# Performance work log

Measured on AMD Instinct MI355X. Metric: run time of the kernel, lower is better.

Reference implementation:

```python
import jax, jax.numpy as jnp
import numpy as np

D_MODEL = 768
NHEAD = 12
D_K = D_MODEL // NHEAD
D_FF = 3072
EPS = 1e-6


def layer_norm(x, a, b):
    # torch LayerNorm here: mean/std over last dim, std is UNBIASED (n-1), eps added to std
    n = x.shape[-1]
    m = jnp.mean(x, axis=-1, keepdims=True)
    var = jnp.sum((x - m) ** 2, axis=-1, keepdims=True) / (n - 1)
    return a * (x - m) / (jnp.sqrt(var) + EPS) + b


def setup_inputs() -> dict:
    key = jax.random.key(0)
    ks = jax.random.split(key, 12)
    B, S = 2, 2048
    s = 1.0 / np.sqrt(D_MODEL)
    inp = {
        'x': jax.random.normal(ks[0], (B, S, D_MODEL), jnp.float32),
        'mask': jnp.ones((B, 1, S), jnp.int32),
        'Wq': jax.random.normal(ks[1], (D_MODEL, D_MODEL), jnp.float32) * s,
        'bq': jnp.zeros((D_MODEL,), jnp.float32),
        'Wk': jax.random.normal(ks[2], (D_MODEL, D_MODEL), jnp.float32) * s,
        'bk': jnp.zeros((D_MODEL,), jnp.float32),
        'Wv': jax.random.normal(ks[3], (D_MODEL, D_MODEL), jnp.float32) * s,
        'bv': jnp.zeros((D_MODEL,), jnp.float32),
        'Wo': jax.random.normal(ks[4], (D_MODEL, D_MODEL), jnp.float32) * s,
        'bo': jnp.zeros((D_MODEL,), jnp.float32),
        'ln1_a': jnp.ones((D_MODEL,), jnp.float32),
        'ln1_b': jnp.zeros((D_MODEL,), jnp.float32),
        'W1': jax.random.normal(ks[5], (D_MODEL, D_FF), jnp.float32) * s,
        'b1': jnp.zeros((D_FF,), jnp.float32),
        'W2': jax.random.normal(ks[6], (D_FF, D_MODEL), jnp.float32) * (1.0 / np.sqrt(D_FF)),
        'b2': jnp.zeros((D_MODEL,), jnp.float32),
        'ln2_a': jnp.ones((D_MODEL,), jnp.float32),
        'ln2_b': jnp.zeros((D_MODEL,), jnp.float32),
    }
    return inp


def reference(x, mask, Wq, bq, Wk, bk, Wv, bv, Wo, bo, ln1_a, ln1_b, W1, b1, W2, b2, ln2_a, ln2_b):
    B, S, _ = x.shape
    # --- sublayer 1: pre-norm self-attention + residual (dropout = eval/no-op) ---
    h = layer_norm(x, ln1_a, ln1_b)
    q = (h @ Wq + bq).reshape(B, S, NHEAD, D_K).transpose(0, 2, 1, 3)  # [B,H,S,Dk]
    k = (h @ Wk + bk).reshape(B, S, NHEAD, D_K).transpose(0, 2, 1, 3)
    v = (h @ Wv + bv).reshape(B, S, NHEAD, D_K).transpose(0, 2, 1, 3)
    scores = jnp.einsum('bhqd,bhkd->bhqk', q, k) / np.sqrt(D_K)  # [B,H,S,S]
    scores = jnp.where(mask[:, None] == 0, jnp.float32(-1e9), scores)
    attn = jax.nn.softmax(scores, axis=-1)
    ctx = jnp.einsum('bhqk,bhkd->bhqd', attn, v)  # [B,H,S,Dk]
    ctx = ctx.transpose(0, 2, 1, 3).reshape(B, S, D_MODEL)
    x = x + (ctx @ Wo + bo)
    # --- sublayer 2: pre-norm FFN + residual ---
    h2 = layer_norm(x, ln2_a, ln2_b)
    ff = jax.nn.relu(h2 @ W1 + b1) @ W2 + b2
    return x + ff
```

## Files before the change

### kernel.cpp

```cpp
#include <hip/hip_runtime.h>
#include <hip/hip_bf16.h>
#include <stdint.h>

#define DM 768
#define DFF 3072
#define NH 12
#define DK 64
#define SS 2048
#define NTOK 4096
#define KCH 2

typedef __hip_bfloat16 bf16;
typedef short bf16x8 __attribute__((ext_vector_type(8)));
typedef float f32x4 __attribute__((ext_vector_type(4)));

#define MFMA16(a, b, c) __builtin_amdgcn_mfma_f32_16x16x32_bf16((a), (b), (c), 0, 0, 0)

#define QSCALE 0.18033688011112042f

#if __has_builtin(__builtin_amdgcn_exp2f)
#define EXP2F(x) __builtin_amdgcn_exp2f(x)
#else
#define EXP2F(x) exp2f(x)
#endif

static __device__ __forceinline__ bf16 f2b(float f) { return __float2bfloat16(f); }
static __device__ __forceinline__ unsigned short f2b_bits(float f) {
    bf16 h = __float2bfloat16(f);
    return *reinterpret_cast<unsigned short*>(&h);
}
static __device__ __forceinline__ float b2f(bf16 h) { return __bfloat162float(h); }

static __device__ __forceinline__ void g2l16(const void* g, void* l) {
    __builtin_amdgcn_global_load_lds(
        (const __attribute__((address_space(1))) unsigned int*)g,
        (__attribute__((address_space(3))) unsigned int*)(uintptr_t)l,
        16, 0, 0);
}

__global__ __launch_bounds__(256) void transpose_all(const float* Wq, const float* Wk,
                                                     const float* Wv, const float* Wo,
                                                     const float* W1, const float* W2,
                                                     bf16* WqT, bf16* WkT, bf16* WvT,
                                                     bf16* WoT, bf16* W1T, bf16* W2T) {
    __shared__ float tile[32][33];
    int id = blockIdx.x;
    const float* W; bf16* WT; int K, N, n0, k0;
    if (id < 2304) {
        int z = id / 576, r = id % 576;
        W  = (z == 0) ? Wq : (z == 1) ? Wk : (z == 2) ? Wv : Wo;
        WT = (z == 0) ? WqT : (z == 1) ? WkT : (z == 2) ? WvT : WoT;
        K = 768; N = 768; n0 = (r % 24) * 32; k0 = (r / 24) * 32;
    } else if (id < 4608) {
        int r = id - 2304; W = W1; WT = W1T;
        K = 768; N = 3072; n0 = (r % 96) * 32; k0 = (r / 96) * 32;
    } else {
        int r = id - 4608; W = W2; WT = W2T;
        K = 3072; N = 768; n0 = (r % 24) * 32; k0 = (r / 24) * 32;
    }
    int tx = threadIdx.x & 31, ty = threadIdx.x >> 5;
#pragma unroll
    for (int r = ty; r < 32; r += 8)
        tile[r][tx] = W[(size_t)(k0 + r) * N + n0 + tx];
    __syncthreads();
#pragma unroll
    for (int r = ty; r < 32; r += 8)
        WT[(size_t)(n0 + r) * K + k0 + tx] = f2b(tile[tx][r]);
}

__global__ __launch_bounds__(256) void ln_fwd(const float* __restrict__ x,
                                              const float* __restrict__ g,
                                              const float* __restrict__ be,
                                              bf16* __restrict__ out) {
    int wid = threadIdx.x >> 6, lane = threadIdx.x & 63;
    int row = blockIdx.x * 4 + wid;
    const float* xr = x + (size_t)row * DM;
    float v[12];
    float s = 0.f;
#pragma unroll
    for (int i = 0; i < 12; ++i) { v[i] = xr[lane + i * 64]; s += v[i]; }
#pragma unroll
    for (int off = 32; off >= 1; off >>= 1) s += __shfl_xor(s, off);
    float mean = s * (1.f / 768.f);
    float s2 = 0.f;
#pragma unroll
    for (int i = 0; i < 12; ++i) { float d = v[i] - mean; s2 += d * d; }
#pragma unroll
    for (int off = 32; off >= 1; off >>= 1) s2 += __shfl_xor(s2, off);
    float rstd = 1.f / (sqrtf(s2 * (1.f / 767.f)) + 1e-6f);
    bf16* orow = out + (size_t)row * DM;
#pragma unroll
    for (int i = 0; i < 12; ++i) {
        int c = lane + i * 64;
        orow[c] = f2b(g[c] * (v[i] - mean) * rstd + be[c]);
    }
}

__device__ __forceinline__ void gemm_core(const bf16* __restrict__ A,
                                          const bf16* __restrict__ BT,
                                          int K, int bm, int bn,
                                          bf16* As, bf16* Bs,
                                          f32x4 acc[4][4]) {
    int tid = threadIdx.x;
    int lane = tid & 63, quad = lane >> 4, lid = lane & 15;
    int wid = tid >> 6;
    int wm = (wid >> 1) * 64, wn = (wid & 1) * 64;
    int s0 = tid, s1 = tid + 256;
    int r0 = s0 >> 2, c0 = (s0 & 3) ^ ((r0 >> 1) & 3);
    int r1 = s1 >> 2, c1 = (s1 & 3) ^ ((r1 >> 1) & 3);
    const bf16* A0 = A + (size_t)(bm + r0) * K + c0 * 8;
    const bf16* A1 = A + (size_t)(bm + r1) * K + c1 * 8;
    const bf16* B0 = BT + (size_t)(bn + r0) * K + c0 * 8;
    const bf16* B1 = BT + (size_t)(bn + r1) * K + c1 * 8;
    int rdc = quad ^ ((lid >> 1) & 3);
    g2l16(A0, As + s0 * 8);
    g2l16(B0, Bs + s0 * 8);
    g2l16(A1, As + s1 * 8);
    g2l16(B1, Bs + s1 * 8);
    for (int k0 = 0; k0 < K; k0 += 32) {
        __syncthreads();
        int cur = (k0 >> 5) & 1;
        if (k0 + 32 < K) {
            int nb = (cur ^ 1) * 4096;
            g2l16(A0 + k0 + 32, As + nb + s0 * 8);
            g2l16(B0 + k0 + 32, Bs + nb + s0 * 8);
            g2l16(A1 + k0 + 32, As + nb + s1 * 8);
            g2l16(B1 + k0 + 32, Bs + nb + s1 * 8);
        }
        const bf16* Ac = As + cur * 4096;
        const bf16* Bc = Bs + cur * 4096;
        bf16x8 af[4], bfr[4];
#pragma unroll
        for (int i = 0; i < 4; ++i) af[i]  = *(const bf16x8*)&Ac[(wm + i * 16 + lid) * 32 + rdc * 8];
#pragma unroll
        for (int j = 0; j < 4; ++j) bfr[j] = *(const bf16x8*)&Bc[(wn + j * 16 + lid) * 32 + rdc * 8];
#pragma unroll
        for (int i = 0; i < 4; ++i)
#pragma unroll
            for (int j = 0; j < 4; ++j)
                acc[i][j] = MFMA16(af[i], bfr[j], acc[i][j]);
    }
}

__global__ __launch_bounds__(256) void gemm_qkv(const bf16* __restrict__ A,
                                                const bf16* __restrict__ WqT,
                                                const bf16* __restrict__ WkT,
                                                const bf16* __restrict__ WvT,
                                                const float* __restrict__ bq,
                                                const float* __restrict__ bk,
                                                const float* __restrict__ bv,
                                                bf16* __restrict__ qb,
                                                bf16* __restrict__ kb,
                                                bf16* __restrict__ vtb) {
    __shared__ bf16 As[2 * 128 * 32];
    __shared__ bf16 Bs[2 * 128 * 32];
    int which = blockIdx.x / 6;
    int bn = (blockIdx.x % 6) * 128;
    int bm = blockIdx.y * 128;
    const bf16* BT = (which == 0) ? WqT : (which == 1) ? WkT : WvT;
    const float* bias = (which == 0) ? bq : (which == 1) ? bk : bv;
    f32x4 acc[4][4] = {};
    gemm_core(A, BT, DM, bm, bn, As, Bs, acc);

    int tid = threadIdx.x, wid = tid >> 6, lane = tid & 63, quad = lane >> 4, lid = lane & 15;
    int wm = (wid >> 1) * 64, wn = (wid & 1) * 64;
    float sc = (which == 0) ? QSCALE : 1.f;
#pragma unroll
    for (int j = 0; j < 4; ++j) {
        int col = bn + wn + j * 16 + lid;
        float bb = bias[col];
        int hh = col >> 6, d = col & 63;
#pragma unroll
        for (int i = 0; i < 4; ++i) {
            int rowbase = bm + wm + i * 16 + quad * 4;
            int b = rowbase >> 11;
            int s0 = rowbase & 2047;
            if (which == 2) {
                ushort4 pk;
                pk.x = f2b_bits(acc[i][j][0] + bb);
                pk.y = f2b_bits(acc[i][j][1] + bb);
                pk.z = f2b_bits(acc[i][j][2] + bb);
                pk.w = f2b_bits(acc[i][j][3] + bb);
                *(ushort4*)&vtb[(((size_t)b * NH + hh) * DK + d) * SS + s0] = pk;
            } else {
                bf16* dst = which ? kb : qb;
#pragma unroll
                for (int r = 0; r < 4; ++r)
                    dst[(((size_t)b * NH + hh) * SS + (s0 + r)) * DK + d] = f2b((acc[i][j][r] + bb) * sc);
            }
        }
    }
}

template <int EPI>
__global__ __launch_bounds__(256) void gemm_ep(const bf16* __restrict__ A,
                                               const bf16* __restrict__ BT,
                                               const float* __restrict__ bias,
                                               const float* __restrict__ res,
                                               void* __restrict__ outp,
                                               int N, int K) {
    __shared__ bf16 As[2 * 128 * 32];
    __shared__ bf16 Bs[2 * 128 * 32];
    int bm = blockIdx.y * 128, bn = blockIdx.x * 128;
    f32x4 acc[4][4] = {};
    gemm_core(A, BT, K, bm, bn, As, Bs, acc);

    int tid = threadIdx.x, wid = tid >> 6, lane = tid & 63, quad = lane >> 4, lid = lane & 15;
    int wm = (wid >> 1) * 64, wn = (wid & 1) * 64;
#pragma unroll
    for (int j = 0; j < 4; ++j) {
        int col = bn + wn + j * 16 + lid;
        float bb = bias[col];
#pragma unroll
        for (int i = 0; i < 4; ++i) {
#pragma unroll
            for (int r = 0; r < 4; ++r) {
                int row = bm + wm + i * 16 + quad * 4 + r;
                float v = acc[i][j][r] + bb;
                if (EPI == 2) {
                    ((float*)outp)[(size_t)row * N + col] = res[(size_t)row * N + col] + v;
                } else {
                    ((bf16*)outp)[(size_t)row * N + col] = f2b(fmaxf(v, 0.f));
                }
            }
        }
    }
}

template <int EPI>
__global__ __launch_bounds__(256) void gemm_ep64(const bf16* __restrict__ A,
                                                 const bf16* __restrict__ BT,
                                                 const float* __restrict__ bias,
                                                 const float* __restrict__ res,
                                                 void* __restrict__ outp,
                                                 int N, int K) {
    __shared__ bf16 As[2 * 64 * 32];
    __shared__ bf16 Bs[2 * 128 * 32];
    int bm = blockIdx.y * 64, bn = blockIdx.x * 128;
    int tid = threadIdx.x, wid = tid >> 6, lane = tid & 63, quad = lane >> 4, lid = lane & 15;
    int wm = (wid >> 1) * 32, wn = (wid & 1) * 64;
    f32x4 acc[2][4] = {};
    int ra = tid >> 2, ca = (tid & 3) ^ ((ra >> 1) & 3);
    int s0 = tid, s1 = tid + 256;
    int rb0 = s0 >> 2, cb0 = (s0 & 3) ^ ((rb0 >> 1) & 3);
    int rb1 = s1 >> 2, cb1 = (s1 & 3) ^ ((rb1 >> 1) & 3);
    const bf16* Ap = A + (size_t)(bm + ra) * K + ca * 8;
    const bf16* B0 = BT + (size_t)(bn + rb0) * K + cb0 * 8;
    const bf16* B1 = BT + (size_t)(bn + rb1) * K + cb1 * 8;
    int rdc = quad ^ ((lid >> 1) & 3);
    g2l16(Ap, As + tid * 8);
    g2l16(B0, Bs + s0 * 8);
    g2l16(B1, Bs + s1 * 8);
    for (int k0 = 0; k0 < K; k0 += 32) {
        __syncthreads();
        int cur = (k0 >> 5) & 1;
        if (k0 + 32 < K) {
            g2l16(Ap + k0 + 32, As + (cur ^ 1) * 2048 + tid * 8);
            g2l16(B0 + k0 + 32, Bs + (cur ^ 1) * 4096 + s0 * 8);
            g2l16(B1 + k0 + 32, Bs + (cur ^ 1) * 4096 + s1 * 8);
        }
        const bf16* Ac = As + cur * 2048;
        const bf16* Bc = Bs + cur * 4096;
        bf16x8 af[2], bfr[4];
#pragma unroll
        for (int i = 0; i < 2; ++i) af[i]  = *(const bf16x8*)&Ac[(wm + i * 16 + lid) * 32 + rdc * 8];
#pragma unroll
        for (int j = 0; j < 4; ++j) bfr[j] = *(const bf16x8*)&Bc[(wn + j * 16 + lid) * 32 + rdc * 8];
#pragma unroll
        for (int i = 0; i < 2; ++i)
#pragma unroll
            for (int j = 0; j < 4; ++j)
                acc[i][j] = MFMA16(af[i], bfr[j], acc[i][j]);
    }
#pragma unroll
    for (int j = 0; j < 4; ++j) {
        int col = bn + wn + j * 16 + lid;
        float bb = bias[col];
#pragma unroll
        for (int i = 0; i < 2; ++i) {
#pragma unroll
            for (int r = 0; r < 4; ++r) {
                int row = bm + wm + i * 16 + quad * 4 + r;
                float v = acc[i][j][r] + bb;
                if (EPI == 2) {
                    ((float*)outp)[(size_t)row * N + col] = res[(size_t)row * N + col] + v;
                } else {
                    ((bf16*)outp)[(size_t)row * N + col] = f2b(fmaxf(v, 0.f));
                }
            }
        }
    }
}

__global__ __launch_bounds__(256) void attn_part(const bf16* __restrict__ qb,
                                                 const bf16* __restrict__ kb,
                                                 const bf16* __restrict__ vtb,
                                                 const int* __restrict__ mask,
                                                 bf16* __restrict__ part,
                                                 float* __restrict__ lws) {
    __shared__ bf16 Ks[2 * 64 * 64];
    __shared__ bf16 VTs[2 * 64 * 64];
    __shared__ bf16 Ps[128 * 72];
    int bh = blockIdx.y;
    int b = bh / NH;
    int q0 = blockIdx.x * 128;
    int kc = blockIdx.z;
    const bf16* Kp = kb  + (size_t)bh * SS * DK;
    const bf16* VT = vtb + (size_t)bh * DK * SS;
    int tid = threadIdx.x, wid = tid >> 6, lane = tid & 63, quad = lane >> 4, lid = lane & 15;

    int s0 = tid, s1 = tid + 256;
    int r0 = s0 >> 3, c0 = (s0 & 7) ^ (r0 & 7);
    int r1 = s1 >> 3, c1 = (s1 & 7) ^ (r1 & 7);

    bf16x8 qf0[2], qf1[2];
#pragma unroll
    for (int u = 0; u < 2; ++u) {
        const bf16* Qrow = qb + ((size_t)bh * SS + q0 + wid * 32 + u * 16 + lid) * DK;
        qf0[u] = *(const bf16x8*)&Qrow[quad * 8];
        qf1[u] = *(const bf16x8*)&Qrow[32 + quad * 8];
    }

    bf16x8 ones;
#pragma unroll
    for (int i = 0; i < 8; ++i) ones[i] = (short)0x3F80;

    int rdc  = quad ^ (lid & 7);
    int rdc2 = rdc ^ 4;
    const int* mrow = mask + b * SS;

    f32x4 accv[2][4] = {};
    f32x4 accl[2] = {};

    int tbeg = kc * (SS / 64 / KCH), tend = (kc + 1) * (SS / 64 / KCH);

    {
        int k0 = tbeg * 64;
        g2l16(Kp + (size_t)(k0 + r0) * DK + c0 * 8, Ks + s0 * 8);
        g2l16(Kp + (size_t)(k0 + r1) * DK + c1 * 8, Ks + s1 * 8);
        g2l16(VT + (size_t)r0 * SS + k0 + c0 * 8, VTs + s0 * 8);
        g2l16(VT + (size_t)r1 * SS + k0 + c1 * 8, VTs + s1 * 8);
    }

    int cur = 0;
    for (int t = tbeg; t < tend; ++t) {
        int k0 = t * 64;
        __syncthreads();
        if (t + 1 < tend) {
            int k0n = (t + 1) * 64;
            int nb = (cur ^ 1) * 4096;
            g2l16(Kp + (size_t)(k0n + r0) * DK + c0 * 8, Ks + nb + s0 * 8);
            g2l16(Kp + (size_t)(k0n + r1) * DK + c1 * 8, Ks + nb + s1 * 8);
            g2l16(VT + (size_t)r0 * SS + k0n + c0 * 8, VTs + nb + s0 * 8);
            g2l16(VT + (size_t)r1 * SS + k0n + c1 * 8, VTs + nb + s1 * 8);
        }
        const bf16* Kc  = Ks  + cur * 4096;
        const bf16* VTc = VTs + cur * 4096;

#pragma unroll
        for (int ns = 0; ns < 4; ++ns) {
            bf16x8 kf0 = *(const bf16x8*)&Kc[(ns * 16 + lid) * 64 + rdc * 8];
            bf16x8 kf1 = *(const bf16x8*)&Kc[(ns * 16 + lid) * 64 + rdc2 * 8];
            int4 mk = *(const int4*)&mrow[k0 + ns * 16 + quad * 4];
#pragma unroll
            for (int u = 0; u < 2; ++u) {
                f32x4 st = {};
                st = MFMA16(kf0, qf0[u], st);
                st = MFMA16(kf1, qf1[u], st);
                float p0 = mk.x ? EXP2F(st[0]) : 0.f;
                float p1 = mk.y ? EXP2F(st[1]) : 0.f;
                float p2 = mk.z ? EXP2F(st[2]) : 0.f;
                float p3 = mk.w ? EXP2F(st[3]) : 0.f;
                __hip_bfloat162 h01 = __float22bfloat162_rn(make_float2(p0, p1));
                __hip_bfloat162 h23 = __float22bfloat162_rn(make_float2(p2, p3));
                uint2 pw;
                pw.x = *(unsigned int*)&h01;
                pw.y = *(unsigned int*)&h23;
                *(uint2*)&Ps[(wid * 32 + u * 16 + lid) * 72 + ns * 16 + quad * 4] = pw;
            }
        }

        bf16x8 pa0[2], pa1[2];
#pragma unroll
        for (int u = 0; u < 2; ++u) {
            pa0[u] = *(const bf16x8*)&Ps[(wid * 32 + u * 16 + lid) * 72 + quad * 8];
            pa1[u] = *(const bf16x8*)&Ps[(wid * 32 + u * 16 + lid) * 72 + 32 + quad * 8];
            accl[u] = MFMA16(pa0[u], ones, accl[u]);
            accl[u] = MFMA16(pa1[u], ones, accl[u]);
        }

#pragma unroll
        for (int ds = 0; ds < 4; ++ds) {
            bf16x8 vf0 = *(const bf16x8*)&VTc[(ds * 16 + lid) * 64 + rdc * 8];
            bf16x8 vf1 = *(const bf16x8*)&VTc[(ds * 16 + lid) * 64 + rdc2 * 8];
#pragma unroll
            for (int u = 0; u < 2; ++u) {
                accv[u][ds] = MFMA16(pa0[u], vf0, accv[u][ds]);
                accv[u][ds] = MFMA16(pa1[u], vf1, accv[u][ds]);
            }
        }
        cur ^= 1;
    }

    bf16* pb = part + ((size_t)kc * (2 * NH) + bh) * DK * SS;
#pragma unroll
    for (int u = 0; u < 2; ++u) {
        if (lid == 0) {
#pragma unroll
            for (int r = 0; r < 4; ++r)
                lws[((size_t)kc * (2 * NH) + bh) * SS + q0 + wid * 32 + u * 16 + quad * 4 + r] = accl[u][r];
        }
        int qbase = q0 + wid * 32 + u * 16 + quad * 4;
#pragma unroll
        for (int ds = 0; ds < 4; ++ds) {
            int d = ds * 16 + lid;
            ushort4 pk;
            pk.x = f2b_bits(accv[u][ds][0]);
            pk.y = f2b_bits(accv[u][ds][1]);
            pk.z = f2b_bits(accv[u][ds][2]);
            pk.w = f2b_bits(accv[u][ds][3]);
            *(ushort4*)&pb[(size_t)d * SS + qbase] = pk;
        }
    }
}

__global__ __launch_bounds__(256) void attn_combine(const bf16* __restrict__ part,
                                                    const float* __restrict__ lws,
                                                    bf16* __restrict__ ctx) {
    __shared__ float tile[64][66];
    __shared__ float linv[64];
    int bh = blockIdx.y;
    int b = bh / NH, h = bh % NH;
    int q0 = blockIdx.x * 64;
    int tid = threadIdx.x;

    if (tid < 64) {
        float l = 0.f;
#pragma unroll
        for (int kc = 0; kc < KCH; ++kc)
            l += lws[((size_t)kc * (2 * NH) + bh) * SS + q0 + tid];
        linv[tid] = 1.f / l;
    }

    int d = tid >> 2, qs = (tid & 3) * 16;
    const bf16* p0 = part + (((size_t)0 * (2 * NH) + bh) * DK + d) * SS + q0 + qs;
    const bf16* p1 = part + (((size_t)1 * (2 * NH) + bh) * DK + d) * SS + q0 + qs;
    bf16x8 a0 = *(const bf16x8*)p0;
    bf16x8 a1 = *(const bf16x8*)(p0 + 8);
    bf16x8 b0 = *(const bf16x8*)p1;
    bf16x8 b1 = *(const bf16x8*)(p1 + 8);
#pragma unroll
    for (int i = 0; i < 8; ++i) {
        tile[d][qs + i]     = b2f(((const bf16*)&a0)[i]) + b2f(((const bf16*)&b0)[i]);
        tile[d][qs + 8 + i] = b2f(((const bf16*)&a1)[i]) + b2f(((const bf16*)&b1)[i]);
    }
    __syncthreads();

    int q = tid >> 2, ds2 = (tid & 3) * 16;
    float rl = linv[q];
    unsigned int wv[8];
#pragma unroll
    for (int i = 0; i < 8; ++i) {
        __hip_bfloat162 hh = __float22bfloat162_rn(
            make_float2(tile[ds2 + 2 * i][q] * rl, tile[ds2 + 2 * i + 1][q] * rl));
        wv[i] = *(unsigned int*)&hh;
    }
    bf16* crow = ctx + (size_t)(b * SS + q0 + q) * DM + h * DK + ds2;
    uint4 u0 = {wv[0], wv[1], wv[2], wv[3]};
    uint4 u1 = {wv[4], wv[5], wv[6], wv[7]};
    *(uint4*)&crow[0] = u0;
    *(uint4*)&crow[8] = u1;
}

extern "C" void kernel_launch(void* const* d_in, const int* in_sizes, int n_in,
                              void* d_out, int out_size, void* d_ws, size_t ws_size,
                              hipStream_t stream) {
    const float* x    = (const float*)d_in[0];
    const int*   mask = (const int*)d_in[1];
    const float* Wq   = (const float*)d_in[2];
    const float* bq   = (const float*)d_in[3];
    const float* Wk   = (const float*)d_in[4];
    const float* bk   = (const float*)d_in[5];
    const float* Wv   = (const float*)d_in[6];
    const float* bv   = (const float*)d_in[7];
    const float* Wo   = (const float*)d_in[8];
    const float* bo   = (const float*)d_in[9];
    const float* ln1a = (const float*)d_in[10];
    const float* ln1b = (const float*)d_in[11];
    const float* W1   = (const float*)d_in[12];
    const float* b1   = (const float*)d_in[13];
    const float* W2   = (const float*)d_in[14];
    const float* b2   = (const float*)d_in[15];
    const float* ln2a = (const float*)d_in[16];
    const float* ln2b = (const float*)d_in[17];
    float* out = (float*)d_out;

    char* w = (char*)d_ws;
    bf16* h   = (bf16*)w; w += (size_t)NTOK * DM * 2;
    bf16* qb  = (bf16*)w; w += (size_t)NTOK * DM * 2;
    bf16* kb  = (bf16*)w; w += (size_t)NTOK * DM * 2;
    bf16* vtb = (bf16*)w; w += (size_t)NTOK * DM * 2;
    bf16* ctx = (bf16*)w; w += (size_t)NTOK * DM * 2;
    bf16* h2  = (bf16*)w; w += (size_t)NTOK * DM * 2;
    bf16* ffa = (bf16*)w; w += (size_t)NTOK * DFF * 2;
    float* x1 = (float*)w; w += (size_t)NTOK * DM * 4;
    bf16* WqT = (bf16*)w; w += (size_t)DM * DM * 2;
    bf16* WkT = (bf16*)w; w += (size_t)DM * DM * 2;
    bf16* WvT = (bf16*)w; w += (size_t)DM * DM * 2;
    bf16* WoT = (bf16*)w; w += (size_t)DM * DM * 2;
    bf16* W1T = (bf16*)w; w += (size_t)DM * DFF * 2;
    bf16* W2T = (bf16*)w; w += (size_t)DM * DFF * 2;

    bf16*  part = ffa;
    float* lws  = x1;

    transpose_all<<<6912, 256, 0, stream>>>(Wq, Wk, Wv, Wo, W1, W2,
                                            WqT, WkT, WvT, WoT, W1T, W2T);

    ln_fwd<<<NTOK / 4, 256, 0, stream>>>(x, ln1a, ln1b, h);
    gemm_qkv<<<dim3(18, 32), 256, 0, stream>>>(h, WqT, WkT, WvT, bq, bk, bv, qb, kb, vtb);
    attn_part<<<dim3(SS / 128, 2 * NH, KCH), 256, 0, stream>>>(qb, kb, vtb, mask, part, lws);
    attn_combine<<<dim3(SS / 64, 2 * NH), 256, 0, stream>>>(part, lws, ctx);
    gemm_ep64<2><<<dim3(6, 64), 256, 0, stream>>>(ctx, WoT, bo, x, (void*)x1, DM, DM);
    ln_fwd<<<NTOK / 4, 256, 0, stream>>>(x1, ln2a, ln2b, h2);
    gemm_ep<3><<<dim3(24, 32), 256, 0, stream>>>(h2, W1T, b1, nullptr, (void*)ffa, DFF, DM);
    gemm_ep64<2><<<dim3(6, 64), 256, 0, stream>>>(ffa, W2T, b2, x1, (void*)out, DM, DFF);
}
```

Before: 291.0 us.

## Split K across two thread halves in gemm_ep64 with shared-memory reduction

Doubles gemm_ep64 block size to 512 threads, with each 256-thread half processing one half of the K dimension in its own double-buffered shared-memory tiles. The second half writes its accumulators into swizzled shared memory and the first half adds them before running the bias/residual epilogue. This is meant to give more waves per output tile on the small Wo and W2 GEMMs (384 blocks), which underfill the GPU. In exchange it adds a reduction step, more shared memory per block, and idle threads during the epilogue.

```diff
diff --git a/kernel.cpp b/kernel.cpp
--- a/kernel.cpp
+++ b/kernel.cpp
@@ -228,34 +228,38 @@
 }
 
 template <int EPI>
-__global__ __launch_bounds__(256) void gemm_ep64(const bf16* __restrict__ A,
+__global__ __launch_bounds__(512) void gemm_ep64(const bf16* __restrict__ A,
                                                  const bf16* __restrict__ BT,
                                                  const float* __restrict__ bias,
                                                  const float* __restrict__ res,
                                                  void* __restrict__ outp,
                                                  int N, int K) {
-    __shared__ bf16 As[2 * 64 * 32];
-    __shared__ bf16 Bs[2 * 128 * 32];
+    __shared__ char smem[49152];
+    int tid = threadIdx.x;
+    int half = tid >> 8, htid = tid & 255;
+    bf16* As = (bf16*)smem + half * 4096;
+    bf16* Bs = (bf16*)(smem + 16384) + half * 8192;
+    int K2 = K >> 1, koff = half * K2;
     int bm = blockIdx.y * 64, bn = blockIdx.x * 128;
-    int tid = threadIdx.x, wid = tid >> 6, lane = tid & 63, quad = lane >> 4, lid = lane & 15;
+    int wid = htid >> 6, lane = tid & 63, quad = lane >> 4, lid = lane & 15;
     int wm = (wid >> 1) * 32, wn = (wid & 1) * 64;
     f32x4 acc[2][4] = {};
-    int ra = tid >> 2, ca = (tid & 3) ^ ((ra >> 1) & 3);
-    int s0 = tid, s1 = tid + 256;
+    int ra = htid >> 2, ca = (htid & 3) ^ ((ra >> 1) & 3);
+    int s0 = htid, s1 = htid + 256;
     int rb0 = s0 >> 2, cb0 = (s0 & 3) ^ ((rb0 >> 1) & 3);
     int rb1 = s1 >> 2, cb1 = (s1 & 3) ^ ((rb1 >> 1) & 3);
-    const bf16* Ap = A + (size_t)(bm + ra) * K + ca * 8;
-    const bf16* B0 = BT + (size_t)(bn + rb0) * K + cb0 * 8;
-    const bf16* B1 = BT + (size_t)(bn + rb1) * K + cb1 * 8;
+    const bf16* Ap = A + (size_t)(bm + ra) * K + koff + ca * 8;
+    const bf16* B0 = BT + (size_t)(bn + rb0) * K + koff + cb0 * 8;
+    const bf16* B1 = BT + (size_t)(bn + rb1) * K + koff + cb1 * 8;
     int rdc = quad ^ ((lid >> 1) & 3);
-    g2l16(Ap, As + tid * 8);
+    g2l16(Ap, As + htid * 8);
     g2l16(B0, Bs + s0 * 8);
     g2l16(B1, Bs + s1 * 8);
-    for (int k0 = 0; k0 < K; k0 += 32) {
+    for (int k0 = 0; k0 < K2; k0 += 32) {
         __syncthreads();
         int cur = (k0 >> 5) & 1;
-        if (k0 + 32 < K) {
-            g2l16(Ap + k0 + 32, As + (cur ^ 1) * 2048 + tid * 8);
+        if (k0 + 32 < K2) {
+            g2l16(Ap + k0 + 32, As + (cur ^ 1) * 2048 + htid * 8);
             g2l16(B0 + k0 + 32, Bs + (cur ^ 1) * 4096 + s0 * 8);
             g2l16(B1 + k0 + 32, Bs + (cur ^ 1) * 4096 + s1 * 8);
         }
@@ -272,20 +276,42 @@
             for (int j = 0; j < 4; ++j)
                 acc[i][j] = MFMA16(af[i], bfr[j], acc[i][j]);
     }
-#pragma unroll
-    for (int j = 0; j < 4; ++j) {
-        int col = bn + wn + j * 16 + lid;
-        float bb = bias[col];
-#pragma unroll
-        for (int i = 0; i < 2; ++i) {
-#pragma unroll
-            for (int r = 0; r < 4; ++r) {
-                int row = bm + wm + i * 16 + quad * 4 + r;
-                float v = acc[i][j][r] + bb;
-                if (EPI == 2) {
-                    ((float*)outp)[(size_t)row * N + col] = res[(size_t)row * N + col] + v;
-                } else {
-                    ((bf16*)outp)[(size_t)row * N + col] = f2b(fmaxf(v, 0.f));
+    __syncthreads();
+    float* red = (float*)smem;
+    if (half == 1) {
+#pragma unroll
+        for (int i = 0; i < 2; ++i)
+#pragma unroll
+            for (int j = 0; j < 4; ++j) {
+                int c = i * 4 + j;
+                *(f32x4*)&red[htid * 32 + ((c ^ (htid & 7)) << 2)] = acc[i][j];
+            }
+    }
+    __syncthreads();
+    if (half == 0) {
+#pragma unroll
+        for (int i = 0; i < 2; ++i)
+#pragma unroll
+            for (int j = 0; j < 4; ++j) {
+                int c = i * 4 + j;
+                f32x4 o = *(const f32x4*)&red[htid * 32 + ((c ^ (htid & 7)) << 2)];
+                acc[i][j] += o;
+            }
+#pragma unroll
+        for (int j = 0; j < 4; ++j) {
+            int col = bn + wn + j * 16 + lid;
+            float bb = bias[col];
+#pragma unroll
+            for (int i = 0; i < 2; ++i) {
+#pragma unroll
+                for (int r = 0; r < 4; ++r) {
+                    int row = bm + wm + i * 16 + quad * 4 + r;
+                    float v = acc[i][j][r] + bb;
+                    if (EPI == 2) {
+                        ((float*)outp)[(size_t)row * N + col] = res[(size_t)row * N + col] + v;
+                    } else {
+                        ((bf16*)outp)[(size_t)row * N + col] = f2b(fmaxf(v, 0.f));
+                    }
                 }
             }
         }
@@ -521,8 +547,8 @@
     gemm_qkv<<<dim3(18, 32), 256, 0, stream>>>(h, WqT, WkT, WvT, bq, bk, bv, qb, kb, vtb);
     attn_part<<<dim3(SS / 128, 2 * NH, KCH), 256, 0, stream>>>(qb, kb, vtb, mask, part, lws);
     attn_combine<<<dim3(SS / 64, 2 * NH), 256, 0, stream>>>(part, lws, ctx);
-    gemm_ep64<2><<<dim3(6, 64), 256, 0, stream>>>(ctx, WoT, bo, x, (void*)x1, DM, DM);
+    gemm_ep64<2><<<dim3(6, 64), 512, 0, stream>>>(ctx, WoT, bo, x, (void*)x1, DM, DM);
     ln_fwd<<<NTOK / 4, 256, 0, stream>>>(x1, ln2a, ln2b, h2);
     gemm_ep<3><<<dim3(24, 32), 256, 0, stream>>>(h2, W1T, b1, nullptr, (void*)ffa, DFF, DM);
-    gemm_ep64<2><<<dim3(6, 64), 256, 0, stream>>>(ffa, W2T, b2, x1, (void*)out, DM, DFF);
-}
+    gemm_ep64<2><<<dim3(6, 64), 512, 0, stream>>>(ffa, W2T, b2, x1, (void*)out, DM, DFF);
+}
```

Result: no change. 288.2 us (-0.9%).

## Fuse first layernorm into transpose launch, retile N=768 GEMMs, skip mask when full

Applied to the files above, without the earlier changes.

Merges the weight transpose/convert kernel and the first layernorm into one launch, with extra blocks handling LN rows. Shrinks the N tile of the two N=768 output GEMMs from 128 to 96 columns, giving 512 blocks instead of 384 for better CU coverage on the mi355x. Adds a block-wide check in attention so fully unmasked key ranges skip the per-tile mask loads and selects. Trade-offs are a lower MFMA-to-load ratio per block in the GEMMs and an extra barrier at the start of attention.

```diff
diff --git a/kernel.cpp b/kernel.cpp
--- a/kernel.cpp
+++ b/kernel.cpp
@@ -38,13 +38,42 @@
         16, 0, 0);
 }
 
-__global__ __launch_bounds__(256) void transpose_all(const float* Wq, const float* Wk,
-                                                     const float* Wv, const float* Wo,
-                                                     const float* W1, const float* W2,
-                                                     bf16* WqT, bf16* WkT, bf16* WvT,
-                                                     bf16* WoT, bf16* W1T, bf16* W2T) {
+__global__ __launch_bounds__(256) void fused_pre(const float* Wq, const float* Wk,
+                                                 const float* Wv, const float* Wo,
+                                                 const float* W1, const float* W2,
+                                                 bf16* WqT, bf16* WkT, bf16* WvT,
+                                                 bf16* WoT, bf16* W1T, bf16* W2T,
+                                                 const float* __restrict__ x,
+                                                 const float* __restrict__ lg,
+                                                 const float* __restrict__ lb,
+                                                 bf16* __restrict__ hout) {
+    int id = blockIdx.x;
+    if (id >= 6912) {
+        int wid = threadIdx.x >> 6, lane = threadIdx.x & 63;
+        int row = (id - 6912) * 4 + wid;
+        const float* xr = x + (size_t)row * DM;
+        float v[12];
+        float s = 0.f;
+#pragma unroll
+        for (int i = 0; i < 12; ++i) { v[i] = xr[lane + i * 64]; s += v[i]; }
+#pragma unroll
+        for (int off = 32; off >= 1; off >>= 1) s += __shfl_xor(s, off);
+        float mean = s * (1.f / 768.f);
+        float s2 = 0.f;
+#pragma unroll
+        for (int i = 0; i < 12; ++i) { float d = v[i] - mean; s2 += d * d; }
+#pragma unroll
+        for (int off = 32; off >= 1; off >>= 1) s2 += __shfl_xor(s2, off);
+        float rstd = 1.f / (sqrtf(s2 * (1.f / 767.f)) + 1e-6f);
+        bf16* orow = hout + (size_t)row * DM;
+#pragma unroll
+        for (int i = 0; i < 12; ++i) {
+            int c = lane + i * 64;
+            orow[c] = f2b(lg[c] * (v[i] - mean) * rstd + lb[c]);
+        }
+        return;
+    }
     __shared__ float tile[32][33];
-    int id = blockIdx.x;
     const float* W; bf16* WT; int K, N, n0, k0;
     if (id < 2304) {
         int z = id / 576, r = id % 576;
@@ -228,18 +257,18 @@
 }
 
 template <int EPI>
-__global__ __launch_bounds__(256) void gemm_ep64(const bf16* __restrict__ A,
+__global__ __launch_bounds__(256) void gemm_ep96(const bf16* __restrict__ A,
                                                  const bf16* __restrict__ BT,
                                                  const float* __restrict__ bias,
                                                  const float* __restrict__ res,
                                                  void* __restrict__ outp,
                                                  int N, int K) {
     __shared__ bf16 As[2 * 64 * 32];
-    __shared__ bf16 Bs[2 * 128 * 32];
-    int bm = blockIdx.y * 64, bn = blockIdx.x * 128;
+    __shared__ bf16 Bs[2 * 96 * 32];
+    int bm = blockIdx.y * 64, bn = blockIdx.x * 96;
     int tid = threadIdx.x, wid = tid >> 6, lane = tid & 63, quad = lane >> 4, lid = lane & 15;
-    int wm = (wid >> 1) * 32, wn = (wid & 1) * 64;
-    f32x4 acc[2][4] = {};
+    int wm = (wid >> 1) * 32, wn = (wid & 1) * 48;
+    f32x4 acc[2][3] = {};
     int ra = tid >> 2, ca = (tid & 3) ^ ((ra >> 1) & 3);
     int s0 = tid, s1 = tid + 256;
     int rb0 = s0 >> 2, cb0 = (s0 & 3) ^ ((rb0 >> 1) & 3);
@@ -248,32 +277,33 @@
     const bf16* B0 = BT + (size_t)(bn + rb0) * K + cb0 * 8;
     const bf16* B1 = BT + (size_t)(bn + rb1) * K + cb1 * 8;
     int rdc = quad ^ ((lid >> 1) & 3);
+    bool doB1 = tid < 128;
     g2l16(Ap, As + tid * 8);
     g2l16(B0, Bs + s0 * 8);
-    g2l16(B1, Bs + s1 * 8);
+    if (doB1) g2l16(B1, Bs + s1 * 8);
     for (int k0 = 0; k0 < K; k0 += 32) {
         __syncthreads();
         int cur = (k0 >> 5) & 1;
         if (k0 + 32 < K) {
             g2l16(Ap + k0 + 32, As + (cur ^ 1) * 2048 + tid * 8);
-            g2l16(B0 + k0 + 32, Bs + (cur ^ 1) * 4096 + s0 * 8);
-            g2l16(B1 + k0 + 32, Bs + (cur ^ 1) * 4096 + s1 * 8);
+            g2l16(B0 + k0 + 32, Bs + (cur ^ 1) * 3072 + s0 * 8);
+            if (doB1) g2l16(B1 + k0 + 32, Bs + (cur ^ 1) * 3072 + s1 * 8);
         }
         const bf16* Ac = As + cur * 2048;
-        const bf16* Bc = Bs + cur * 4096;
-        bf16x8 af[2], bfr[4];
+        const bf16* Bc = Bs + cur * 3072;
+        bf16x8 af[2], bfr[3];
 #pragma unroll
         for (int i = 0; i < 2; ++i) af[i]  = *(const bf16x8*)&Ac[(wm + i * 16 + lid) * 32 + rdc * 8];
 #pragma unroll
-        for (int j = 0; j < 4; ++j) bfr[j] = *(const bf16x8*)&Bc[(wn + j * 16 + lid) * 32 + rdc * 8];
+        for (int j = 0; j < 3; ++j) bfr[j] = *(const bf16x8*)&Bc[(wn + j * 16 + lid) * 32 + rdc * 8];
 #pragma unroll
         for (int i = 0; i < 2; ++i)
 #pragma unroll
-            for (int j = 0; j < 4; ++j)
+            for (int j = 0; j < 3; ++j)
                 acc[i][j] = MFMA16(af[i], bfr[j], acc[i][j]);
     }
 #pragma unroll
-    for (int j = 0; j < 4; ++j) {
+    for (int j = 0; j < 3; ++j) {
         int col = bn + wn + j * 16 + lid;
         float bb = bias[col];
 #pragma unroll
@@ -313,6 +343,17 @@
     int r0 = s0 >> 3, c0 = (s0 & 7) ^ (r0 & 7);
     int r1 = s1 >> 3, c1 = (s1 & 7) ^ (r1 & 7);
 
+    const int* mrow = mask + b * SS;
+    int tbeg = kc * (SS / 64 / KCH), tend = (kc + 1) * (SS / 64 / KCH);
+
+    int myfull;
+    {
+        const int4* m4 = (const int4*)(mrow + tbeg * 64);
+        int4 mm = m4[tid];
+        myfull = (mm.x != 0) & (mm.y != 0) & (mm.z != 0) & (mm.w != 0);
+    }
+    int blockfull = __syncthreads_and(myfull);
+
     bf16x8 qf0[2], qf1[2];
 #pragma unroll
     for (int u = 0; u < 2; ++u) {
@@ -327,12 +368,9 @@
 
     int rdc  = quad ^ (lid & 7);
     int rdc2 = rdc ^ 4;
-    const int* mrow = mask + b * SS;
 
     f32x4 accv[2][4] = {};
     f32x4 accl[2] = {};
-
-    int tbeg = kc * (SS / 64 / KCH), tend = (kc + 1) * (SS / 64 / KCH);
 
     {
         int k0 = tbeg * 64;
@@ -361,16 +399,24 @@
         for (int ns = 0; ns < 4; ++ns) {
             bf16x8 kf0 = *(const bf16x8*)&Kc[(ns * 16 + lid) * 64 + rdc * 8];
             bf16x8 kf1 = *(const bf16x8*)&Kc[(ns * 16 + lid) * 64 + rdc2 * 8];
-            int4 mk = *(const int4*)&mrow[k0 + ns * 16 + quad * 4];
 #pragma unroll
             for (int u = 0; u < 2; ++u) {
                 f32x4 st = {};
                 st = MFMA16(kf0, qf0[u], st);
                 st = MFMA16(kf1, qf1[u], st);
-                float p0 = mk.x ? EXP2F(st[0]) : 0.f;
-                float p1 = mk.y ? EXP2F(st[1]) : 0.f;
-                float p2 = mk.z ? EXP2F(st[2]) : 0.f;
-                float p3 = mk.w ? EXP2F(st[3]) : 0.f;
+                float p0, p1, p2, p3;
+                if (blockfull) {
+                    p0 = EXP2F(st[0]);
+                    p1 = EXP2F(st[1]);
+                    p2 = EXP2F(st[2]);
+                    p3 = EXP2F(st[3]);
+                } else {
+                    int4 mk = *(const int4*)&mrow[k0 + ns * 16 + quad * 4];
+                    p0 = mk.x ? EXP2F(st[0]) : 0.f;
+                    p1 = mk.y ? EXP2F(st[1]) : 0.f;
+                    p2 = mk.z ? EXP2F(st[2]) : 0.f;
+                    p3 = mk.w ? EXP2F(st[3]) : 0.f;
+                }
                 __hip_bfloat162 h01 = __float22bfloat162_rn(make_float2(p0, p1));
                 __hip_bfloat162 h23 = __float22bfloat162_rn(make_float2(p2, p3));
                 uint2 pw;
@@ -514,15 +560,14 @@
     bf16*  part = ffa;
     float* lws  = x1;
 
-    transpose_all<<<6912, 256, 0, stream>>>(Wq, Wk, Wv, Wo, W1, W2,
-                                            WqT, WkT, WvT, WoT, W1T, W2T);
-
-    ln_fwd<<<NTOK / 4, 256, 0, stream>>>(x, ln1a, ln1b, h);
+    fused_pre<<<6912 + NTOK / 4, 256, 0, stream>>>(Wq, Wk, Wv, Wo, W1, W2,
+                                                   WqT, WkT, WvT, WoT, W1T, W2T,
+                                                   x, ln1a, ln1b, h);
     gemm_qkv<<<dim3(18, 32), 256, 0, stream>>>(h, WqT, WkT, WvT, bq, bk, bv, qb, kb, vtb);
     attn_part<<<dim3(SS / 128, 2 * NH, KCH), 256, 0, stream>>>(qb, kb, vtb, mask, part, lws);
     attn_combine<<<dim3(SS / 64, 2 * NH), 256, 0, stream>>>(part, lws, ctx);
-    gemm_ep64<2><<<dim3(6, 64), 256, 0, stream>>>(ctx, WoT, bo, x, (void*)x1, DM, DM);
+    gemm_ep96<2><<<dim3(8, 64), 256, 0, stream>>>(ctx, WoT, bo, x, (void*)x1, DM, DM);
     ln_fwd<<<NTOK / 4, 256, 0, stream>>>(x1, ln2a, ln2b, h2);
     gemm_ep<3><<<dim3(24, 32), 256, 0, stream>>>(h2, W1T, b1, nullptr, (void*)ffa, DFF, DM);
-    gemm_ep64<2><<<dim3(6, 64), 256, 0, stream>>>(ffa, W2T, b2, x1, (void*)out, DM, DFF);
-}
+    gemm_ep96<2><<<dim3(8, 64), 256, 0, stream>>>(ffa, W2T, b2, x1, (void*)out, DM, DFF);
+}
```

Measured after the change: 287.0 us. About the same (-1.4%).
